# Kernel optimization log

Measured on AMD Instinct MI355X. Metric: run time of the kernel, lower is better.

## Reference

```python
import jax, jax.numpy as jnp
import numpy as np

H = W = 64
ALPHA = 1.0
BETA = 100.0
LIMB_PAIRS = np.array([[0,1],[1,2],[2,3],[0,4],[4,5],[5,6],[0,7],[7,8],[8,9],[9,10],
                       [8,11],[11,12],[12,13],[8,14],[14,15],[15,16]])
P0 = LIMB_PAIRS[:, 0]
P1 = LIMB_PAIRS[:, 1]
_last = {}
for _l, _j in enumerate(P0):
    _last[int(_j)] = _l
J0 = np.array(list(_last.keys()))   # unique proximal joints
L0 = np.array(list(_last.values())) # last limb writing to each joint


def make_kernel(h, w, alpha):
    # replicates: coords = stack(meshgrid(arange(2h-1), arange(2w-1))).transpose(1,2) (h==w)
    ii, jj = jnp.meshgrid(jnp.arange(2 * h - 1), jnp.arange(2 * w - 1), indexing='ij')
    ker = jnp.stack([h - jj, w - ii], axis=0).astype(jnp.float32)  # (2, 2h-1, 2w-1)
    dist = jnp.linalg.norm(ker, axis=0, keepdims=True)
    dist = dist.at[0, h, w].set(1.0)
    return ker / dist ** (1.0 + alpha)


def corr_full(x, k):
    # x: (N, Cin, h, w); k: (Cout, Cin, 2h-1, 2w-1); 'same' correlation with pad h-1/w-1
    h, w = x.shape[-2:]
    return jax.lax.conv_general_dilated(x, k, (1, 1), ((h - 1, h - 1), (w - 1, w - 1)))


def heatmap_std(x, di=False):
    axes = (3, 4, 5) if di else (3, 4)
    return jnp.std(x, axis=axes, keepdims=True, ddof=1)


def heatmap_normalize(x, std, di=False):
    return x * std / (heatmap_std(x, di) + 1e-6)


def l2norm(v, axis):
    return v / jnp.maximum(jnp.linalg.norm(v, axis=axis, keepdims=True), 1e-12)


def soft_argmax(hm, beta):
    # hm: ... x h x w -> ... x 2 with (row_coord, col_coord) as in the torch code
    h, w = hm.shape[-2:]
    p = jax.nn.softmax(hm.reshape(hm.shape[:-2] + (-1,)) * beta, axis=-1).reshape(hm.shape)
    rows = jnp.arange(h, dtype=p.dtype)[:, None]
    cols = jnp.arange(w, dtype=p.dtype)[None, :]
    norm = p.sum((-2, -1))
    kp_x = (p * rows).sum((-2, -1)) / norm
    kp_y = (p * cols).sum((-2, -1)) / norm
    return jnp.stack((kp_x, kp_y), axis=-1)


def scale_pts(pts, image_shape, h, w):
    return jnp.stack((pts[..., 0] * image_shape[1] / w,
                      pts[..., 1] * image_shape[0] / h), axis=-1)


def cofix_forward(heatmaps, fields, Ps, Rs, Cs, image_shape, confs, vth1, vth2, pth1, pth2):
    bs, nv, nL, _, h, w = fields.shape
    nJ = heatmaps.shape[2]
    K = make_kernel(h, w, ALPHA)  # (2, 2h-1, 2w-1)

    heatmaps = heatmaps - jnp.mean(heatmaps, axis=(3, 4), keepdims=True)
    std_hm = heatmap_std(heatmaps, di=False)
    std_df = heatmap_std(fields, di=True)

    Hs = heatmaps[:, :, P1] - heatmaps[:, :, P0]  # (bs, nv, nL, h, w)
    # conv3d(kernel1, flipped Hs) == 'same' correlation of Hs with spatially-reversed K
    k1 = K[:, ::-1, ::-1][:, None]  # (2, 1, 2h-1, 2w-1)
    convs = corr_full(Hs.reshape(-1, 1, h, w), k1).reshape(bs, nv, nL, 2, h, w)

    coef = jax.nn.relu(jnp.sum(convs * fields[..., :2, :, :], axis=3, keepdims=True))
    fields_new = fields * coef

    fnorm = jnp.linalg.norm(fields, axis=3, keepdims=True)
    lvecs = l2norm(jnp.sum(fnorm * fields, axis=(4, 5)), axis=3)
    lpts = scale_pts(soft_argmax(fnorm[:, :, :, 0], BETA), image_shape, h, w)

    fnorm_new = jnp.linalg.norm(fields_new, axis=3, keepdims=True)
    lvecs_new = l2norm(jnp.sum(fnorm_new * fields_new, axis=(4, 5)), axis=3)
    lpts_new = scale_pts(soft_argmax(fnorm_new[:, :, :, 0], BETA), image_shape, h, w)

    # original code computes vec_selection(...) then overwrites: delta[:] = 0
    delta = jnp.zeros((bs, nv, nL, 1), dtype=heatmaps.dtype)
    comb_v = delta * lvecs_new + (1 - delta) * lvecs
    comb_p = delta * lpts_new + (1 - delta) * lpts

    d6 = delta[..., None, None]
    fields_c = heatmap_normalize(fields * (1 - d6) + fields_new * d6, std_df, di=True)

    # conv2d(kernel2, fields) then output spatial flip == 'same' correlation with K
    k2 = K[None]  # (1, 2, 2h-1, 2w-1)
    fds2jts = corr_full(fields_c[..., :2, :, :].reshape(-1, 2, h, w), k2)
    fds2jts = fds2jts.reshape(bs, nv, nL, h, w)
    prox_ = jax.nn.relu(-fds2jts)
    dist_ = jax.nn.relu(fds2jts)

    hms_new = heatmaps.at[:, :, J0].set(heatmaps[:, :, J0] * prox_[:, :, L0])
    hms_new = hms_new.at[:, :, P1].set(hms_new[:, :, P1] * dist_)
    hms_new = heatmap_normalize(hms_new, std_hm, di=False)

    kps = scale_pts(soft_argmax(heatmaps, BETA), image_shape, h, w)[..., None]
    kps_new = scale_pts(soft_argmax(hms_new, BETA), image_shape, h, w)[..., None]
    kps_new = jnp.where(jnp.isnan(kps_new), kps, kps_new)

    # sed_selection (reconstructed): keep refined kps where joint conf is high and
    # the refinement displacement is small.
    confs_j = confs[:, :, nL:]
    disp = jnp.linalg.norm((kps_new - kps)[..., 0], axis=-1)  # (bs, nv, nJ)
    sel = ((confs_j > pth1) & (disp < pth2)).astype(kps.dtype)[..., None, None]
    kps_combined = sel * kps_new + (1 - sel) * kps

    return kps_combined, comb_v, comb_p, fields_new, hms_new


def setup_inputs() -> dict:
    key = jax.random.key(0)
    ks = jax.random.split(key, 6)
    bs, nv, nJ, nL = 4, 4, 17, 16
    return {
        'heatmaps': jax.random.uniform(ks[0], (bs, nv, nJ, H, W), jnp.float32),
        'fields': jax.random.normal(ks[1], (bs, nv, nL, 3, H, W), jnp.float32),
        'Ps': jax.random.normal(ks[2], (bs, nv, 3, 4), jnp.float32),
        'Rs': jax.random.normal(ks[3], (bs, nv, 3, 3), jnp.float32),
        'Cs': jax.random.normal(ks[4], (bs, nv, 3, 1), jnp.float32),
        'image_shape': jnp.array([384, 384], jnp.int32),
        'confs': jax.random.uniform(ks[5], (bs, nv, nL + nJ), jnp.float32),
        'vth1': 0.5, 'vth2': 0.5, 'pth1': 0.1, 'pth2': 20.0,
    }


def reference(heatmaps, fields, Ps, Rs, Cs, image_shape, confs, vth1, vth2, pth1, pth2):
    return cofix_forward(heatmaps, fields, Ps, Rs, Cs, image_shape, confs,
                         vth1, vth2, pth1, pth2)
```

## Files before the change

kernel.cpp:

```cpp
#include <hip/hip_runtime.h>
#include <math.h>

#define TPB 1024
#define HTPB 256
#define NPIX 4096
#define NJ 17
#define NL 16
static constexpr float kBeta = 100.0f;
static constexpr float S2H = 0.70710678118654752f;

#define O_KPS 0
#define O_CV 544
#define O_CP 1312
#define O_FN 1824
#define O_HM 3147552
#define W_FDS 0
#define W_MEAN 1048576
#define W_STD 1048848
#define W_SF 1049120
#define W_W1 1049376
#define W_W2 1082144

__device__ __constant__ int c_P0[16] = {0,1,2,0,4,5,0,7,8,9,8,11,12,8,14,15};
__device__ __constant__ int c_P1[16] = {1,2,3,4,5,6,7,8,9,10,11,12,13,14,15,16};
__device__ __constant__ int c_proxL[17] = {6,1,2,-1,4,5,-1,7,13,9,-1,11,12,-1,14,15,-1};
__device__ __constant__ int c_distL[17] = {-1,0,1,2,3,4,5,6,7,8,9,10,11,12,13,14,15};

using cplx = float2;
__device__ inline cplx cadd(cplx a, cplx b){ return {a.x+b.x, a.y+b.y}; }
__device__ inline cplx csub(cplx a, cplx b){ return {a.x-b.x, a.y-b.y}; }
__device__ inline cplx cmul(cplx a, cplx w){ return {a.x*w.x - a.y*w.y, a.x*w.y + a.y*w.x}; }
__device__ inline cplx cmulc(cplx a, cplx w){ return {a.x*w.x + a.y*w.y, a.y*w.x - a.x*w.y}; }

__device__ inline void wsync(){
  asm volatile("s_waitcnt lgkmcnt(0)" ::: "memory");
}

__device__ __constant__ float2 W128BR[8] = {
  {1.f,0.f},
  {0.98078528040323044913f,-0.19509032201612826785f},
  {0.99518472667219688624f,-0.09801714032956060199f},
  {0.95694033573220886494f,-0.29028467725446236764f},
  {0.99879545620517239271f,-0.04906767432741801425f},
  {0.97003125319454399260f,-0.24298017990326388995f},
  {0.98917650996478097345f,-0.14673047445536175166f},
  {0.94154406518302077841f,-0.33688985339222005069f}
};
__device__ __constant__ float2 W16BR[8] = {
  {1.f,0.f},
  {0.f,-1.f},
  {0.70710678118654752440f,-0.70710678118654752440f},
  {-0.70710678118654752440f,-0.70710678118654752440f},
  {0.92387953251128675613f,-0.38268343236508977173f},
  {-0.38268343236508977173f,-0.92387953251128675613f},
  {0.38268343236508977173f,-0.92387953251128675613f},
  {-0.92387953251128675613f,-0.38268343236508977173f}
};

__device__ inline void bf8_tail(cplx t0, cplx t1, cplx t2, cplx t3,
                                cplx t4, cplx t5, cplx t6, cplx t7, cplx x[8]){
  cplx u0=cadd(t0,t2), u2=csub(t0,t2);
  cplx u1=cadd(t1,t3), d13=csub(t1,t3);
  cplx u3={d13.y,-d13.x};
  cplx u4=cadd(t4,t6), u6=csub(t4,t6);
  cplx u5=cadd(t5,t7), d57=csub(t5,t7);
  cplx u7={d57.y,-d57.x};
  x[0]=cadd(u0,u1); x[1]=csub(u0,u1);
  x[2]=cadd(u2,u3); x[3]=csub(u2,u3);
  x[4]=cadd(u4,u5); x[5]=csub(u4,u5);
  x[6]=cadd(u6,u7); x[7]=csub(u6,u7);
}
__device__ inline void bf8_fwd(cplx x[8]){
  cplx t0=cadd(x[0],x[4]), d4=csub(x[0],x[4]);
  cplx t1=cadd(x[1],x[5]), d5=csub(x[1],x[5]);
  cplx t2=cadd(x[2],x[6]), d6=csub(x[2],x[6]);
  cplx t3=cadd(x[3],x[7]), d7=csub(x[3],x[7]);
  cplx t5={S2H*(d5.x+d5.y), S2H*(d5.y-d5.x)};
  cplx t6={d6.y,-d6.x};
  cplx t7={S2H*(d7.y-d7.x), -S2H*(d7.x+d7.y)};
  bf8_tail(t0,t1,t2,t3,d4,t5,t6,t7,x);
}
__device__ inline void bf8_fwd_z(cplx x[8]){
  cplx t5={S2H*(x[1].x+x[1].y), S2H*(x[1].y-x[1].x)};
  cplx t6={x[2].y,-x[2].x};
  cplx t7={S2H*(x[3].y-x[3].x), -S2H*(x[3].x+x[3].y)};
  bf8_tail(x[0],x[1],x[2],x[3],x[0],t5,t6,t7,x);
}
__device__ inline void bf8_inv(cplx y[8]){
  cplx u0=cadd(y[0],y[1]), u1=csub(y[0],y[1]);
  cplx u2=cadd(y[2],y[3]), u3=csub(y[2],y[3]);
  cplx u4=cadd(y[4],y[5]), u5=csub(y[4],y[5]);
  cplx u6=cadd(y[6],y[7]), u7=csub(y[6],y[7]);
  cplx t0=cadd(u0,u2), t2=csub(u0,u2);
  cplx iu3={-u3.y,u3.x};
  cplx t1=cadd(u1,iu3), t3=csub(u1,iu3);
  cplx t4=cadd(u4,u6), t6=csub(u4,u6);
  cplx iu7={-u7.y,u7.x};
  cplx t5=cadd(u5,iu7), t7=csub(u5,iu7);
  y[0]=cadd(t0,t4); y[4]=csub(t0,t4);
  cplx w5={S2H*(t5.x-t5.y), S2H*(t5.x+t5.y)};
  y[1]=cadd(t1,w5); y[5]=csub(t1,w5);
  cplx w6={-t6.y,t6.x};
  y[2]=cadd(t2,w6); y[6]=csub(t2,w6);
  cplx w7={-S2H*(t7.x+t7.y), S2H*(t7.x-t7.y)};
  y[3]=cadd(t3,w7); y[7]=csub(t3,w7);
}

__device__ inline void fft16_fwd(cplx z[16]){
  cplx e[8], o[8];
  #pragma unroll
  for (int t=0;t<8;t++){ e[t]=z[2*t]; o[t]=z[2*t+1]; }
  bf8_fwd(e); bf8_fwd(o);
  #pragma unroll
  for (int p=0;p<8;p++){
    cplx vo = cmul(o[p], W16BR[p]);
    z[2*p]   = cadd(e[p], vo);
    z[2*p+1] = csub(e[p], vo);
  }
}
__device__ inline void fft16_inv(cplx z[16]){
  cplx e[8], o[8];
  #pragma unroll
  for (int p=0;p<8;p++){
    cplx a=z[2*p], b=z[2*p+1];
    e[p] = cadd(a,b);
    o[p] = cmulc(csub(a,b), W16BR[p]);
  }
  bf8_inv(e); bf8_inv(o);
  #pragma unroll
  for (int t=0;t<8;t++){ z[2*t]=e[t]; z[2*t+1]=o[t]; }
}

__device__ inline void twchainA(const cplx* TW, int j, cplx A[8]){
  cplx W1 = TW[j];
  cplx W2 = cmul(W1,W1);
  cplx W4 = cmul(W2,W2);
  cplx W6 = cmul(W4,W2);
  A[0] = {1.f,0.f}; A[1] = W4; A[2] = W2; A[3] = W6;
  A[4] = W1; A[5] = cmul(W4,W1); A[6] = cmul(W2,W1); A[7] = cmul(W6,W1);
}

__device__ inline int PH(int y, int m){
  return (y<<6) | ((m ^ ((y&7)*9) ^ ((y>>3)&7)) & 63);
}

template<bool ZT>
__device__ inline void row_s1_f(float4* S4, const cplx* TW, int L, int m){
  cplx xe[8], xo[8];
  #pragma unroll
  for (int t=0; t<(ZT?4:8); t++){
    float4 v = S4[PH(L, m+8*t)];
    xe[t]={v.x,v.y}; xo[t]={v.z,v.w};
  }
  if (ZT){ bf8_fwd_z(xe); bf8_fwd_z(xo); } else { bf8_fwd(xe); bf8_fwd(xo); }
  cplx A[8]; twchainA(TW, 2*m, A);
  #pragma unroll
  for (int p=0;p<8;p++){
    cplx B = cmul(A[p], W128BR[p]);
    cplx ve = cmul(xe[p], A[p]);
    cplx vo = cmul(xo[p], B);
    S4[PH(L, m+8*p)] = {ve.x, ve.y, vo.x, vo.y};
  }
}
__device__ inline void row_s1_i(float4* S4, const cplx* TW, int L, int m){
  cplx xe[8], xo[8];
  #pragma unroll
  for (int p=0;p<8;p++){
    float4 v = S4[PH(L, m+8*p)];
    xe[p]={v.x,v.y}; xo[p]={v.z,v.w};
  }
  cplx A[8]; twchainA(TW, 2*m, A);
  #pragma unroll
  for (int p=0;p<8;p++){
    cplx B = cmul(A[p], W128BR[p]);
    xe[p] = cmulc(xe[p], A[p]);
    xo[p] = cmulc(xo[p], B);
  }
  bf8_inv(xe); bf8_inv(xo);
  #pragma unroll
  for (int t=0;t<4;t++)
    S4[PH(L, m+8*t)] = {xe[t].x, xe[t].y, xo[t].x, xo[t].y};
}
__device__ inline void row_s2_f(float4* S4, int L, int jb){
  cplx z[16];
  #pragma unroll
  for (int k=0;k<8;k++){
    float4 v = S4[PH(L, jb*8+k)];
    z[2*k]={v.x,v.y}; z[2*k+1]={v.z,v.w};
  }
  fft16_fwd(z);
  #pragma unroll
  for (int k=0;k<8;k++)
    S4[PH(L, jb*8+k)] = {z[2*k].x, z[2*k].y, z[2*k+1].x, z[2*k+1].y};
}
__device__ inline void row_s2_i(float4* S4, int L, int jb){
  cplx z[16];
  #pragma unroll
  for (int k=0;k<8;k++){
    float4 v = S4[PH(L, jb*8+k)];
    z[2*k]={v.x,v.y}; z[2*k+1]={v.z,v.w};
  }
  fft16_inv(z);
  #pragma unroll
  for (int k=0;k<8;k++)
    S4[PH(L, jb*8+k)] = {z[2*k].x, z[2*k].y, z[2*k+1].x, z[2*k+1].y};
}
template<bool ZT>
__device__ inline void col_s1_f(float4* S4, const cplx* TW, int yj, int sc){
  cplx xe[8], xo[8];
  #pragma unroll
  for (int t=0; t<(ZT?4:8); t++){
    float4 v = S4[PH(yj+16*t, sc)];
    xe[t]={v.x,v.y}; xo[t]={v.z,v.w};
  }
  if (ZT){ bf8_fwd_z(xe); bf8_fwd_z(xo); } else { bf8_fwd(xe); bf8_fwd(xo); }
  cplx A[8]; twchainA(TW, yj, A);
  #pragma unroll
  for (int p=0;p<8;p++){
    cplx ve = cmul(xe[p], A[p]);
    cplx vo = cmul(xo[p], A[p]);
    S4[PH(yj+16*p, sc)] = {ve.x, ve.y, vo.x, vo.y};
  }
}
__device__ inline void col_s1_i(float4* S4, const cplx* TW, int yj, int sc){
  cplx xe[8], xo[8];
  #pragma unroll
  for (int p=0;p<8;p++){
    float4 v = S4[PH(yj+16*p, sc)];
    xe[p]={v.x,v.y}; xo[p]={v.z,v.w};
  }
  cplx A[8]; twchainA(TW, yj, A);
  #pragma unroll
  for (int p=0;p<8;p++){
    xe[p] = cmulc(xe[p], A[p]);
    xo[p] = cmulc(xo[p], A[p]);
  }
  bf8_inv(xe); bf8_inv(xo);
  #pragma unroll
  for (int t=0;t<4;t++)
    S4[PH(yj+16*t, sc)] = {xe[t].x, xe[t].y, xo[t].x, xo[t].y};
}

__device__ inline float wred(float v){
  #pragma unroll
  for (int o=32;o;o>>=1) v += __shfl_xor(v, o, 64);
  return v;
}
__device__ inline float wredmax(float v){
  #pragma unroll
  for (int o=32;o;o>>=1) v = fmaxf(v, __shfl_xor(v, o, 64));
  return v;
}
template<int NW>
__device__ inline void bred3(float& a, float& b, float& c,
                             float* s0, float* s1, float* s2, int tid){
  a = wred(a); b = wred(b); c = wred(c);
  const int w = tid >> 6;
  if ((tid & 63) == 0){ s0[w]=a; s1[w]=b; s2[w]=c; }
  __syncthreads();
  if (tid == 0){
    float A=0.f, B=0.f, C=0.f;
    #pragma unroll
    for (int i=0;i<NW;i++){ A+=s0[i]; B+=s1[i]; C+=s2[i]; }
    s0[0]=A; s1[0]=B; s2[0]=C;
  }
  __syncthreads();
  a = s0[0]; b = s1[0]; c = s2[0];
  __syncthreads();
}
template<int NW>
__device__ inline float bredmax(float v, float* s0, int tid){
  v = wredmax(v);
  const int w = tid >> 6;
  if ((tid & 63) == 0) s0[w] = v;
  __syncthreads();
  if (tid == 0){
    float M = s0[0];
    #pragma unroll
    for (int i=1;i<NW;i++) M = fmaxf(M, s0[i]);
    s0[0] = M;
  }
  __syncthreads();
  const float r = s0[0];
  __syncthreads();
  return r;
}

__device__ inline cplx wval(int r, int c, int which){
  const int dy = (r<64)? r : r-128;
  const int dx = (c<64)? c : c-128;
  float a, b;
  if (which==0){ a = 1.f-(float)dy; b = 1.f-(float)dx; }
  else         { a = 1.f+(float)dy; b = 1.f+(float)dx; }
  const float den = a*a + b*b;
  if (r==64 || c==64 || den<=0.f) return {0.f,0.f};
  const float inv = 1.f/den;
  return {a*inv, -b*inv};
}

__global__ __launch_bounds__(TPB,4) void pre_kernel(const float* __restrict__ heat,
                                                    const float* __restrict__ fields,
                                                    const int* __restrict__ ishape,
                                                    float* __restrict__ mean_hm,
                                                    float* __restrict__ std_hm,
                                                    float* __restrict__ sf,
                                                    float* __restrict__ W1,
                                                    float* __restrict__ W2,
                                                    float* __restrict__ out){
  __shared__ float4 S4[8192];
  __shared__ cplx TW[128];
  __shared__ float sA[16], sB[16], sC[16];
  const int tid = threadIdx.x;
  const int wv = tid >> 6, lane = tid & 63;
  const int blk = blockIdx.x;
  if (blk < 2){
    const int which = blk;
    if (tid < 128){
      float s, c;
      sincosf(-6.283185307179586f * (float)tid / 128.0f, &s, &c);
      TW[tid] = {c, s};
    }
    for (int s = tid; s < 8192; s += TPB){
      const int y = s>>6, m = s&63;
      const cplx v0 = wval(y, 2*m, which);
      const cplx v1 = wval(y, 2*m+1, which);
      S4[PH(y, m)] = {v0.x, v0.y, v1.x, v1.y};
    }
    __syncthreads();
    {
      const int L = 8*wv + (lane>>3), m = lane&7;
      row_s1_f<false>(S4, TW, L, m);
      wsync();
      row_s2_f(S4, L, m);
    }
    __syncthreads();
    {
      const int yj = lane & 15, sc = 4*wv + (lane>>4);
      col_s1_f<false>(S4, TW, yj, sc);
      wsync();
      cplx* Sc = (cplx*)S4;
      const int c = 8*wv + (lane&7), r = lane>>3;
      cplx z[16];
      #pragma unroll
      for (int i=0;i<16;i++)
        z[i] = Sc[2*PH(16*r+i, c>>1) + (c&1)];
      fft16_fwd(z);
      cplx* Wo = (cplx*)((which==0)?W1:W2);
      const float scl = 1.0f / 16384.0f;
      #pragma unroll
      for (int i=0;i<16;i++) Wo[(16*r+i)*128 + c] = {z[i].x*scl, z[i].y*scl};
    }
  } else if (blk < 274){
    const int n = blk - 2;
    const float4* p4 = (const float4*)(heat + (size_t)n * NPIX);
    const float4 x = p4[tid];
    float s = x.x+x.y+x.z+x.w;
    float s2 = x.x*x.x + x.y*x.y + x.z*x.z + x.w*x.w;
    float d = 0.0f;
    bred3<16>(s, s2, d, sA, sB, sC, tid);
    if (tid == 0){
      const float mean = s / 4096.0f;
      const float var = (s2 - s*mean) / 4095.0f;
      mean_hm[n] = mean;
      std_hm[n] = sqrtf(fmaxf(var, 0.0f));
    }
  } else {
    const int m = blk - 274;
    const float4* F4 = (const float4*)(fields + (size_t)m * 3 * NPIX);
    const float4 f0 = F4[tid], f1 = F4[1024+tid], f2 = F4[2048+tid];
    const float f0a[4] = {f0.x,f0.y,f0.z,f0.w};
    const float f1a[4] = {f1.x,f1.y,f1.z,f1.w};
    const float f2a[4] = {f2.x,f2.y,f2.z,f2.w};
    float fn[4];
    float s1 = 0.0f, s2 = 0.0f;
    float a0 = 0.0f, a1 = 0.0f, a2 = 0.0f;
    #pragma unroll
    for (int j = 0; j < 4; j++){
      s1 += f0a[j]+f1a[j]+f2a[j];
      s2 += f0a[j]*f0a[j]+f1a[j]*f1a[j]+f2a[j]*f2a[j];
      const float nn = sqrtf(f0a[j]*f0a[j] + f1a[j]*f1a[j] + f2a[j]*f2a[j]);
      fn[j] = nn;
      a0 += nn*f0a[j]; a1 += nn*f1a[j]; a2 += nn*f2a[j];
    }
    {
      float t1 = s1, t2 = s2, t3 = 0.0f;
      bred3<16>(t1, t2, t3, sA, sB, sC, tid);
      if (tid == 0){
        const float var = (t2 - t1*t1/12288.0f) / 12287.0f;
        const float sd = sqrtf(fmaxf(var, 0.0f));
        sf[m] = sd / (sd + 1e-6f);
      }
    }
    bred3<16>(a0, a1, a2, sA, sB, sC, tid);
    float mx = fmaxf(fmaxf(fn[0],fn[1]), fmaxf(fn[2],fn[3]));
    mx = bredmax<16>(mx, sA, tid);
    float Sm = 0.0f, Sx = 0.0f, Sy = 0.0f;
    #pragma unroll
    for (int j = 0; j < 4; j++){
      const int px = tid*4 + j;
      const float e = expf(kBeta * (fn[j] - mx));
      Sm += e; Sx += e * (float)(px>>6); Sy += e * (float)(px&63);
    }
    bred3<16>(Sm, Sx, Sy, sA, sB, sC, tid);
    if (tid == 0){
      float nrm = sqrtf(a0*a0 + a1*a1 + a2*a2);
      nrm = fmaxf(nrm, 1e-12f);
      out[O_CV + m*3 + 0] = a0/nrm;
      out[O_CV + m*3 + 1] = a1/nrm;
      out[O_CV + m*3 + 2] = a2/nrm;
      const float sxs = (float)ishape[1] / 64.0f;
      const float sys = (float)ishape[0] / 64.0f;
      out[O_CP + m*2 + 0] = Sx/Sm * sxs;
      out[O_CP + m*2 + 1] = Sy/Sm * sys;
    }
  }
}

__global__ __launch_bounds__(TPB,4) void conv_kernel(const float* __restrict__ heat,
                                                     const float* __restrict__ mean_hm,
                                                     const float* __restrict__ fields,
                                                     const float* __restrict__ sf,
                                                     const float* __restrict__ W1g,
                                                     const float* __restrict__ W2g,
                                                     float* __restrict__ out_fn,
                                                     float* __restrict__ fds){
  __shared__ float4 S4[8192];
  __shared__ cplx TW[128];
  const int tid = threadIdx.x;
  const int wv = tid >> 6, lane = tid & 63;
  const int n = blockIdx.x;
  const bool is2 = (n < 256);
  const int m_img = is2 ? n : (n - 256);
  if (tid < 128){
    float s, c;
    sincosf(-6.283185307179586f * (float)tid / 128.0f, &s, &c);
    TW[tid] = {c, s};
  }
  const float* f = fields + (size_t)m_img * 3 * NPIX;
  {
    const int y = tid >> 4, x4 = (tid & 15) << 2;
    const int i = (y << 6) + x4;
    const int m = (tid & 15) << 1;
    if (!is2){
      const int bv = m_img >> 4, l = m_img & 15;
      const int j1 = bv*NJ + c_P1[l], j0 = bv*NJ + c_P0[l];
      const float dm = mean_hm[j1] - mean_hm[j0];
      const float4 a = *(const float4*)(heat + (size_t)j1*NPIX + i);
      const float4 b = *(const float4*)(heat + (size_t)j0*NPIX + i);
      S4[PH(y, m  )] = {a.x-b.x-dm, 0.f, a.y-b.y-dm, 0.f};
      S4[PH(y, m+1)] = {a.z-b.z-dm, 0.f, a.w-b.w-dm, 0.f};
    } else {
      const float4 A = *(const float4*)(f + NPIX + i);
      const float4 B = *(const float4*)(f + i);
      S4[PH(y, m  )] = {A.x, B.x, A.y, B.y};
      S4[PH(y, m+1)] = {A.z, B.z, A.w, B.w};
    }
  }
  __syncthreads();
  if (wv < 8){
    const int L = 8*wv + (lane>>3), m = lane&7;
    row_s1_f<true>(S4, TW, L, m);
    wsync();
    row_s2_f(S4, L, m);
  }
  __syncthreads();
  {
    const cplx* Wg = (const cplx*)(is2 ? W2g : W1g);
    const int c = 8*wv + (lane&7), r = lane>>3;
    cplx wvv[16];
    #pragma unroll
    for (int i=0;i<16;i++) wvv[i] = Wg[(16*r+i)*128 + c];
    const int yj = lane & 15, sc = 4*wv + (lane>>4);
    col_s1_f<true>(S4, TW, yj, sc);
    wsync();
    {
      cplx* Sc = (cplx*)S4;
      cplx z[16];
      int ad[16];
      #pragma unroll
      for (int i=0;i<16;i++){
        ad[i] = 2*PH(16*r+i, c>>1) + (c&1);
        z[i] = Sc[ad[i]];
      }
      fft16_fwd(z);
      #pragma unroll
      for (int i=0;i<16;i++) z[i] = cmul(z[i], wvv[i]);
      fft16_inv(z);
      #pragma unroll
      for (int i=0;i<16;i++) Sc[ad[i]] = z[i];
    }
    wsync();
    col_s1_i(S4, TW, yj, sc);
  }
  __syncthreads();
  if (wv < 8){
    const int L = 8*wv + (lane>>3), m = lane&7;
    row_s2_i(S4, L, m);
    wsync();
    row_s1_i(S4, TW, L, m);
  }
  __syncthreads();
  {
    const int y = tid >> 4, x4 = (tid & 15) << 2;
    const int i = (y << 6) + x4;
    const int m = (tid & 15) << 1;
    const float4 va = S4[PH(y, m)];
    const float4 vb = S4[PH(y, m+1)];
    if (!is2){
      float* o = out_fn + (size_t)m_img * 3 * NPIX;
      const float4 f0 = *(const float4*)(f + i);
      const float4 f1 = *(const float4*)(f + NPIX + i);
      const float4 f2 = *(const float4*)(f + 2*NPIX + i);
      const float c0[4] = {-va.y, -va.w, -vb.y, -vb.w};
      const float c1[4] = { va.x,  va.z,  vb.x,  vb.z};
      const float f0a[4] = {f0.x,f0.y,f0.z,f0.w};
      const float f1a[4] = {f1.x,f1.y,f1.z,f1.w};
      const float f2a[4] = {f2.x,f2.y,f2.z,f2.w};
      float o0[4], o1[4], o2[4];
      #pragma unroll
      for (int j=0;j<4;j++){
        const float cf = fmaxf(0.f, c0[j]*f0a[j] + c1[j]*f1a[j]);
        o0[j] = f0a[j]*cf; o1[j] = f1a[j]*cf; o2[j] = f2a[j]*cf;
      }
      *(float4*)(o + i)          = {o0[0],o0[1],o0[2],o0[3]};
      *(float4*)(o + NPIX + i)   = {o1[0],o1[1],o1[2],o1[3]};
      *(float4*)(o + 2*NPIX + i) = {o2[0],o2[1],o2[2],o2[3]};
    } else {
      const float sc2 = sf[m_img];
      float* o = fds + (size_t)m_img * NPIX;
      *(float4*)(o + i) = {va.x*sc2, va.z*sc2, vb.x*sc2, vb.z*sc2};
    }
  }
}

__global__ __launch_bounds__(HTPB) void hms_kernel(const float* __restrict__ heat,
                                                   const float* __restrict__ mean_hm,
                                                   const float* __restrict__ std_hm,
                                                   const float* __restrict__ fds,
                                                   const float* __restrict__ confs,
                                                   const int* __restrict__ ishape,
                                                   const float* __restrict__ pth1p,
                                                   const float* __restrict__ pth2p,
                                                   float* __restrict__ out){
  __shared__ float sA[4], sB[4], sC[4];
  const int tid = threadIdx.x;
  const int idx = blockIdx.x;
  const int bv = idx / NJ, j = idx % NJ;
  const float4* hp4 = (const float4*)(heat + (size_t)idx * NPIX);
  const float mh = mean_hm[idx];
  const int pl = c_proxL[j], dl = c_distL[j];
  const float4* fp4 = (pl >= 0) ? (const float4*)(fds + (size_t)(bv*NL + pl) * NPIX) : nullptr;
  const float4* fd4 = (dl >= 0) ? (const float4*)(fds + (size_t)(bv*NL + dl) * NPIX) : nullptr;
  float ho[16], hn[16];
  float s = 0.0f, s2 = 0.0f, dummy = 0.0f;
  #pragma unroll
  for (int i = 0; i < 4; i++){
    const int u = tid + i*HTPB;
    const float4 h4 = hp4[u];
    const float hv[4] = {h4.x-mh, h4.y-mh, h4.z-mh, h4.w-mh};
    float pv[4] = {1.f,1.f,1.f,1.f};
    if (pl >= 0){
      const float4 p4 = fp4[u];
      pv[0] = fmaxf(0.f,-p4.x); pv[1] = fmaxf(0.f,-p4.y);
      pv[2] = fmaxf(0.f,-p4.z); pv[3] = fmaxf(0.f,-p4.w);
    }
    float dv[4] = {1.f,1.f,1.f,1.f};
    if (dl >= 0){
      const float4 d4 = fd4[u];
      dv[0] = fmaxf(0.f,d4.x); dv[1] = fmaxf(0.f,d4.y);
      dv[2] = fmaxf(0.f,d4.z); dv[3] = fmaxf(0.f,d4.w);
    }
    #pragma unroll
    for (int k=0;k<4;k++){
      ho[4*i+k] = hv[k];
      const float m = hv[k]*pv[k]*dv[k];
      hn[4*i+k] = m;
      s += m; s2 += m*m;
    }
  }
  bred3<4>(s, s2, dummy, sA, sB, sC, tid);
  const float var = (s2 - s*s/4096.0f) / 4095.0f;
  const float sdn = sqrtf(fmaxf(var, 0.0f));
  const float scale = std_hm[idx] / (sdn + 1e-6f);
  float4* ohm4 = (float4*)(out + O_HM + (size_t)idx * NPIX);
  #pragma unroll
  for (int i = 0; i < 4; i++){
    #pragma unroll
    for (int k=0;k<4;k++) hn[4*i+k] *= scale;
    ohm4[tid + i*HTPB] = {hn[4*i], hn[4*i+1], hn[4*i+2], hn[4*i+3]};
  }
  float mo = -1e30f, mn = -1e30f;
  #pragma unroll
  for (int i = 0; i < 16; i++){ mo = fmaxf(mo, ho[i]); mn = fmaxf(mn, hn[i]); }
  mo = bredmax<4>(mo, sA, tid);
  mn = bredmax<4>(mn, sA, tid);
  float So = 0.0f, Sxo = 0.0f, Syo = 0.0f;
  float Sn = 0.0f, Sxn = 0.0f, Syn = 0.0f;
  #pragma unroll
  for (int i = 0; i < 16; i++){
    const int px = (tid + (i>>2)*HTPB)*4 + (i&3);
    const float y = (float)(px >> 6), x = (float)(px & 63);
    const float eo = expf(kBeta * (ho[i] - mo));
    So += eo; Sxo += eo*y; Syo += eo*x;
    const float en = expf(kBeta * (hn[i] - mn));
    Sn += en; Sxn += en*y; Syn += en*x;
  }
  bred3<4>(So, Sxo, Syo, sA, sB, sC, tid);
  bred3<4>(Sn, Sxn, Syn, sA, sB, sC, tid);
  if (tid == 0){
    const float sxs = (float)ishape[1] / 64.0f;
    const float sys = (float)ishape[0] / 64.0f;
    const float kxo = Sxo/So * sxs, kyo = Syo/So * sys;
    float kxn = Sxn/Sn * sxs, kyn = Syn/Sn * sys;
    if (kxn != kxn) kxn = kxo;
    if (kyn != kyn) kyn = kyo;
    const float ddx = kxn - kxo, ddy = kyn - kyo;
    const float disp = sqrtf(ddx*ddx + ddy*ddy);
    const float conf = confs[bv*(NL+NJ) + NL + j];
    const bool sel = (conf > pth1p[0]) && (disp < pth2p[0]);
    out[O_KPS + idx*2 + 0] = sel ? kxn : kxo;
    out[O_KPS + idx*2 + 1] = sel ? kyn : kyo;
  }
}

extern "C" void kernel_launch(void* const* d_in, const int* in_sizes, int n_in,
                              void* d_out, int out_size, void* d_ws, size_t ws_size,
                              hipStream_t stream) {
  const float* heat   = (const float*)d_in[0];
  const float* fields = (const float*)d_in[1];
  const int*   ishape = (const int*)d_in[5];
  const float* confs  = (const float*)d_in[6];
  const float* pth1   = (const float*)d_in[9];
  const float* pth2   = (const float*)d_in[10];
  float* out = (float*)d_out;
  float* ws = (float*)d_ws;
  float* fds     = ws + W_FDS;
  float* mean_hm = ws + W_MEAN;
  float* std_hm  = ws + W_STD;
  float* sf      = ws + W_SF;
  float* W1      = ws + W_W1;
  float* W2      = ws + W_W2;

  hipLaunchKernelGGL(pre_kernel, dim3(530), dim3(TPB), 0, stream,
                     heat, fields, ishape, mean_hm, std_hm, sf, W1, W2, out);
  hipLaunchKernelGGL(conv_kernel, dim3(512), dim3(TPB), 0, stream,
                     heat, mean_hm, fields, sf, W1, W2, out + O_FN, fds);
  hipLaunchKernelGGL(hms_kernel, dim3(272), dim3(HTPB), 0, stream,
                     heat, mean_hm, std_hm, fds, confs, ishape, pth1, pth2, out);
}
```

Before: 142.8 us.

## Fold per-image statistics into conv and heatmap kernels, shrink pre-kernel

Removes the heatmap mean/std and field statistics work from the first kernel and recomputes them inside the consumers: conv_kernel computes the difference mean and the field std via block reductions, and takes over the field-norm soft-argmax and combined-vector outputs. hms_kernel computes its own heatmap mean and std with an extra reduction pass. The first kernel now only builds the two FFT weight grids in two blocks, which shortens the serial critical path and drops the workspace round trips. In exchange conv and hms blocks carry extra reductions and syncs, and the z-channel of each field is loaded one more time.

```diff
diff --git a/kernel.cpp b/kernel.cpp
--- a/kernel.cpp
+++ b/kernel.cpp
@@ -15,9 +15,6 @@
 #define O_FN 1824
 #define O_HM 3147552
 #define W_FDS 0
-#define W_MEAN 1048576
-#define W_STD 1048848
-#define W_SF 1049120
 #define W_W1 1049376
 #define W_W2 1082144
 
@@ -252,6 +249,23 @@
   return v;
 }
 template<int NW>
+__device__ inline float bred1(float v, float* s0, int tid){
+  v = wred(v);
+  const int w = tid >> 6;
+  if ((tid & 63) == 0) s0[w] = v;
+  __syncthreads();
+  if (tid == 0){
+    float A = 0.f;
+    #pragma unroll
+    for (int i=0;i<NW;i++) A += s0[i];
+    s0[0] = A;
+  }
+  __syncthreads();
+  const float r = s0[0];
+  __syncthreads();
+  return r;
+}
+template<int NW>
 __device__ inline void bred3(float& a, float& b, float& c,
                              float* s0, float* s1, float* s2, int tid){
   a = wred(a); b = wred(b); c = wred(c);
@@ -298,134 +312,60 @@
   return {a*inv, -b*inv};
 }
 
-__global__ __launch_bounds__(TPB,4) void pre_kernel(const float* __restrict__ heat,
-                                                    const float* __restrict__ fields,
-                                                    const int* __restrict__ ishape,
-                                                    float* __restrict__ mean_hm,
-                                                    float* __restrict__ std_hm,
-                                                    float* __restrict__ sf,
-                                                    float* __restrict__ W1,
-                                                    float* __restrict__ W2,
-                                                    float* __restrict__ out){
+__global__ __launch_bounds__(TPB,4) void prep_kernel(float* __restrict__ W1,
+                                                     float* __restrict__ W2){
+  __shared__ float4 S4[8192];
+  __shared__ cplx TW[128];
+  const int tid = threadIdx.x;
+  const int wvx = tid >> 6, lane = tid & 63;
+  const int which = blockIdx.x;
+  if (tid < 128){
+    float s, c;
+    sincosf(-6.283185307179586f * (float)tid / 128.0f, &s, &c);
+    TW[tid] = {c, s};
+  }
+  for (int s = tid; s < 8192; s += TPB){
+    const int y = s>>6, m = s&63;
+    const cplx v0 = wval(y, 2*m, which);
+    const cplx v1 = wval(y, 2*m+1, which);
+    S4[PH(y, m)] = {v0.x, v0.y, v1.x, v1.y};
+  }
+  __syncthreads();
+  {
+    const int L = 8*wvx + (lane>>3), m = lane&7;
+    row_s1_f<false>(S4, TW, L, m);
+    wsync();
+    row_s2_f(S4, L, m);
+  }
+  __syncthreads();
+  {
+    const int yj = lane & 15, sc = 4*wvx + (lane>>4);
+    col_s1_f<false>(S4, TW, yj, sc);
+    wsync();
+    cplx* Sc = (cplx*)S4;
+    const int c = 8*wvx + (lane&7), r = lane>>3;
+    cplx z[16];
+    #pragma unroll
+    for (int i=0;i<16;i++)
+      z[i] = Sc[2*PH(16*r+i, c>>1) + (c&1)];
+    fft16_fwd(z);
+    cplx* Wo = (cplx*)((which==0)?W1:W2);
+    const float scl = 1.0f / 16384.0f;
+    #pragma unroll
+    for (int i=0;i<16;i++) Wo[(16*r+i)*128 + c] = {z[i].x*scl, z[i].y*scl};
+  }
+}
+
+__global__ __launch_bounds__(TPB,4) void conv_kernel(const float* __restrict__ heat,
+                                                     const float* __restrict__ fields,
+                                                     const float* __restrict__ W1g,
+                                                     const float* __restrict__ W2g,
+                                                     const int* __restrict__ ishape,
+                                                     float* __restrict__ out,
+                                                     float* __restrict__ fds){
   __shared__ float4 S4[8192];
   __shared__ cplx TW[128];
   __shared__ float sA[16], sB[16], sC[16];
-  const int tid = threadIdx.x;
-  const int wv = tid >> 6, lane = tid & 63;
-  const int blk = blockIdx.x;
-  if (blk < 2){
-    const int which = blk;
-    if (tid < 128){
-      float s, c;
-      sincosf(-6.283185307179586f * (float)tid / 128.0f, &s, &c);
-      TW[tid] = {c, s};
-    }
-    for (int s = tid; s < 8192; s += TPB){
-      const int y = s>>6, m = s&63;
-      const cplx v0 = wval(y, 2*m, which);
-      const cplx v1 = wval(y, 2*m+1, which);
-      S4[PH(y, m)] = {v0.x, v0.y, v1.x, v1.y};
-    }
-    __syncthreads();
-    {
-      const int L = 8*wv + (lane>>3), m = lane&7;
-      row_s1_f<false>(S4, TW, L, m);
-      wsync();
-      row_s2_f(S4, L, m);
-    }
-    __syncthreads();
-    {
-      const int yj = lane & 15, sc = 4*wv + (lane>>4);
-      col_s1_f<false>(S4, TW, yj, sc);
-      wsync();
-      cplx* Sc = (cplx*)S4;
-      const int c = 8*wv + (lane&7), r = lane>>3;
-      cplx z[16];
-      #pragma unroll
-      for (int i=0;i<16;i++)
-        z[i] = Sc[2*PH(16*r+i, c>>1) + (c&1)];
-      fft16_fwd(z);
-      cplx* Wo = (cplx*)((which==0)?W1:W2);
-      const float scl = 1.0f / 16384.0f;
-      #pragma unroll
-      for (int i=0;i<16;i++) Wo[(16*r+i)*128 + c] = {z[i].x*scl, z[i].y*scl};
-    }
-  } else if (blk < 274){
-    const int n = blk - 2;
-    const float4* p4 = (const float4*)(heat + (size_t)n * NPIX);
-    const float4 x = p4[tid];
-    float s = x.x+x.y+x.z+x.w;
-    float s2 = x.x*x.x + x.y*x.y + x.z*x.z + x.w*x.w;
-    float d = 0.0f;
-    bred3<16>(s, s2, d, sA, sB, sC, tid);
-    if (tid == 0){
-      const float mean = s / 4096.0f;
-      const float var = (s2 - s*mean) / 4095.0f;
-      mean_hm[n] = mean;
-      std_hm[n] = sqrtf(fmaxf(var, 0.0f));
-    }
-  } else {
-    const int m = blk - 274;
-    const float4* F4 = (const float4*)(fields + (size_t)m * 3 * NPIX);
-    const float4 f0 = F4[tid], f1 = F4[1024+tid], f2 = F4[2048+tid];
-    const float f0a[4] = {f0.x,f0.y,f0.z,f0.w};
-    const float f1a[4] = {f1.x,f1.y,f1.z,f1.w};
-    const float f2a[4] = {f2.x,f2.y,f2.z,f2.w};
-    float fn[4];
-    float s1 = 0.0f, s2 = 0.0f;
-    float a0 = 0.0f, a1 = 0.0f, a2 = 0.0f;
-    #pragma unroll
-    for (int j = 0; j < 4; j++){
-      s1 += f0a[j]+f1a[j]+f2a[j];
-      s2 += f0a[j]*f0a[j]+f1a[j]*f1a[j]+f2a[j]*f2a[j];
-      const float nn = sqrtf(f0a[j]*f0a[j] + f1a[j]*f1a[j] + f2a[j]*f2a[j]);
-      fn[j] = nn;
-      a0 += nn*f0a[j]; a1 += nn*f1a[j]; a2 += nn*f2a[j];
-    }
-    {
-      float t1 = s1, t2 = s2, t3 = 0.0f;
-      bred3<16>(t1, t2, t3, sA, sB, sC, tid);
-      if (tid == 0){
-        const float var = (t2 - t1*t1/12288.0f) / 12287.0f;
-        const float sd = sqrtf(fmaxf(var, 0.0f));
-        sf[m] = sd / (sd + 1e-6f);
-      }
-    }
-    bred3<16>(a0, a1, a2, sA, sB, sC, tid);
-    float mx = fmaxf(fmaxf(fn[0],fn[1]), fmaxf(fn[2],fn[3]));
-    mx = bredmax<16>(mx, sA, tid);
-    float Sm = 0.0f, Sx = 0.0f, Sy = 0.0f;
-    #pragma unroll
-    for (int j = 0; j < 4; j++){
-      const int px = tid*4 + j;
-      const float e = expf(kBeta * (fn[j] - mx));
-      Sm += e; Sx += e * (float)(px>>6); Sy += e * (float)(px&63);
-    }
-    bred3<16>(Sm, Sx, Sy, sA, sB, sC, tid);
-    if (tid == 0){
-      float nrm = sqrtf(a0*a0 + a1*a1 + a2*a2);
-      nrm = fmaxf(nrm, 1e-12f);
-      out[O_CV + m*3 + 0] = a0/nrm;
-      out[O_CV + m*3 + 1] = a1/nrm;
-      out[O_CV + m*3 + 2] = a2/nrm;
-      const float sxs = (float)ishape[1] / 64.0f;
-      const float sys = (float)ishape[0] / 64.0f;
-      out[O_CP + m*2 + 0] = Sx/Sm * sxs;
-      out[O_CP + m*2 + 1] = Sy/Sm * sys;
-    }
-  }
-}
-
-__global__ __launch_bounds__(TPB,4) void conv_kernel(const float* __restrict__ heat,
-                                                     const float* __restrict__ mean_hm,
-                                                     const float* __restrict__ fields,
-                                                     const float* __restrict__ sf,
-                                                     const float* __restrict__ W1g,
-                                                     const float* __restrict__ W2g,
-                                                     float* __restrict__ out_fn,
-                                                     float* __restrict__ fds){
-  __shared__ float4 S4[8192];
-  __shared__ cplx TW[128];
   const int tid = threadIdx.x;
   const int wv = tid >> 6, lane = tid & 63;
   const int n = blockIdx.x;
@@ -437,31 +377,41 @@
     TW[tid] = {c, s};
   }
   const float* f = fields + (size_t)m_img * 3 * NPIX;
-  {
-    const int y = tid >> 4, x4 = (tid & 15) << 2;
-    const int i = (y << 6) + x4;
-    const int m = (tid & 15) << 1;
-    if (!is2){
-      const int bv = m_img >> 4, l = m_img & 15;
-      const int j1 = bv*NJ + c_P1[l], j0 = bv*NJ + c_P0[l];
-      const float dm = mean_hm[j1] - mean_hm[j0];
-      const float4 a = *(const float4*)(heat + (size_t)j1*NPIX + i);
-      const float4 b = *(const float4*)(heat + (size_t)j0*NPIX + i);
-      S4[PH(y, m  )] = {a.x-b.x-dm, 0.f, a.y-b.y-dm, 0.f};
-      S4[PH(y, m+1)] = {a.z-b.z-dm, 0.f, a.w-b.w-dm, 0.f};
-    } else {
-      const float4 A = *(const float4*)(f + NPIX + i);
-      const float4 B = *(const float4*)(f + i);
-      S4[PH(y, m  )] = {A.x, B.x, A.y, B.y};
-      S4[PH(y, m+1)] = {A.z, B.z, A.w, B.w};
-    }
+  const int y = tid >> 4, x4 = (tid & 15) << 2;
+  const int i = (y << 6) + x4;
+  const int m = (tid & 15) << 1;
+  float sf_loc = 0.0f;
+  if (!is2){
+    const int bv = m_img >> 4, l = m_img & 15;
+    const int j1 = bv*NJ + c_P1[l], j0 = bv*NJ + c_P0[l];
+    const float4 a = *(const float4*)(heat + (size_t)j1*NPIX + i);
+    const float4 b = *(const float4*)(heat + (size_t)j0*NPIX + i);
+    const float d0=a.x-b.x, d1=a.y-b.y, d2=a.z-b.z, d3=a.w-b.w;
+    const float dm = bred1<16>(d0+d1+d2+d3, sA, tid) * (1.0f/4096.0f);
+    S4[PH(y, m  )] = {d0-dm, 0.f, d1-dm, 0.f};
+    S4[PH(y, m+1)] = {d2-dm, 0.f, d3-dm, 0.f};
+  } else {
+    const float4 A = *(const float4*)(f + NPIX + i);
+    const float4 B = *(const float4*)(f + i);
+    const float4 C = *(const float4*)(f + 2*NPIX + i);
+    S4[PH(y, m  )] = {A.x, B.x, A.y, B.y};
+    S4[PH(y, m+1)] = {A.z, B.z, A.w, B.w};
+    float s1 = A.x+A.y+A.z+A.w + B.x+B.y+B.z+B.w + C.x+C.y+C.z+C.w;
+    float s2 = A.x*A.x+A.y*A.y+A.z*A.z+A.w*A.w
+             + B.x*B.x+B.y*B.y+B.z*B.z+B.w*B.w
+             + C.x*C.x+C.y*C.y+C.z*C.z+C.w*C.w;
+    float d = 0.0f;
+    bred3<16>(s1, s2, d, sA, sB, sC, tid);
+    const float var = (s2 - s1*s1/12288.0f) / 12287.0f;
+    const float sd = sqrtf(fmaxf(var, 0.0f));
+    sf_loc = sd / (sd + 1e-6f);
   }
   __syncthreads();
   if (wv < 8){
-    const int L = 8*wv + (lane>>3), m = lane&7;
-    row_s1_f<true>(S4, TW, L, m);
+    const int L = 8*wv + (lane>>3), mm = lane&7;
+    row_s1_f<true>(S4, TW, L, mm);
     wsync();
-    row_s2_f(S4, L, m);
+    row_s2_f(S4, L, mm);
   }
   __syncthreads();
   {
@@ -469,7 +419,7 @@
     const int c = 8*wv + (lane&7), r = lane>>3;
     cplx wvv[16];
     #pragma unroll
-    for (int i=0;i<16;i++) wvv[i] = Wg[(16*r+i)*128 + c];
+    for (int k=0;k<16;k++) wvv[k] = Wg[(16*r+k)*128 + c];
     const int yj = lane & 15, sc = 4*wv + (lane>>4);
     col_s1_f<true>(S4, TW, yj, sc);
     wsync();
@@ -478,64 +428,81 @@
       cplx z[16];
       int ad[16];
       #pragma unroll
-      for (int i=0;i<16;i++){
-        ad[i] = 2*PH(16*r+i, c>>1) + (c&1);
-        z[i] = Sc[ad[i]];
+      for (int k=0;k<16;k++){
+        ad[k] = 2*PH(16*r+k, c>>1) + (c&1);
+        z[k] = Sc[ad[k]];
       }
       fft16_fwd(z);
       #pragma unroll
-      for (int i=0;i<16;i++) z[i] = cmul(z[i], wvv[i]);
+      for (int k=0;k<16;k++) z[k] = cmul(z[k], wvv[k]);
       fft16_inv(z);
       #pragma unroll
-      for (int i=0;i<16;i++) Sc[ad[i]] = z[i];
+      for (int k=0;k<16;k++) Sc[ad[k]] = z[k];
     }
     wsync();
     col_s1_i(S4, TW, yj, sc);
   }
   __syncthreads();
   if (wv < 8){
-    const int L = 8*wv + (lane>>3), m = lane&7;
-    row_s2_i(S4, L, m);
+    const int L = 8*wv + (lane>>3), mm = lane&7;
+    row_s2_i(S4, L, mm);
     wsync();
-    row_s1_i(S4, TW, L, m);
-  }
-  __syncthreads();
-  {
-    const int y = tid >> 4, x4 = (tid & 15) << 2;
-    const int i = (y << 6) + x4;
-    const int m = (tid & 15) << 1;
-    const float4 va = S4[PH(y, m)];
-    const float4 vb = S4[PH(y, m+1)];
-    if (!is2){
-      float* o = out_fn + (size_t)m_img * 3 * NPIX;
-      const float4 f0 = *(const float4*)(f + i);
-      const float4 f1 = *(const float4*)(f + NPIX + i);
-      const float4 f2 = *(const float4*)(f + 2*NPIX + i);
-      const float c0[4] = {-va.y, -va.w, -vb.y, -vb.w};
-      const float c1[4] = { va.x,  va.z,  vb.x,  vb.z};
-      const float f0a[4] = {f0.x,f0.y,f0.z,f0.w};
-      const float f1a[4] = {f1.x,f1.y,f1.z,f1.w};
-      const float f2a[4] = {f2.x,f2.y,f2.z,f2.w};
-      float o0[4], o1[4], o2[4];
-      #pragma unroll
-      for (int j=0;j<4;j++){
-        const float cf = fmaxf(0.f, c0[j]*f0a[j] + c1[j]*f1a[j]);
-        o0[j] = f0a[j]*cf; o1[j] = f1a[j]*cf; o2[j] = f2a[j]*cf;
-      }
-      *(float4*)(o + i)          = {o0[0],o0[1],o0[2],o0[3]};
-      *(float4*)(o + NPIX + i)   = {o1[0],o1[1],o1[2],o1[3]};
-      *(float4*)(o + 2*NPIX + i) = {o2[0],o2[1],o2[2],o2[3]};
-    } else {
-      const float sc2 = sf[m_img];
-      float* o = fds + (size_t)m_img * NPIX;
-      *(float4*)(o + i) = {va.x*sc2, va.z*sc2, vb.x*sc2, vb.z*sc2};
+    row_s1_i(S4, TW, L, mm);
+  }
+  __syncthreads();
+  const float4 va = S4[PH(y, m)];
+  const float4 vb = S4[PH(y, m+1)];
+  if (!is2){
+    float* o = out + O_FN + (size_t)m_img * 3 * NPIX;
+    const float4 f0 = *(const float4*)(f + i);
+    const float4 f1 = *(const float4*)(f + NPIX + i);
+    const float4 f2 = *(const float4*)(f + 2*NPIX + i);
+    const float c0[4] = {-va.y, -va.w, -vb.y, -vb.w};
+    const float c1[4] = { va.x,  va.z,  vb.x,  vb.z};
+    const float f0a[4] = {f0.x,f0.y,f0.z,f0.w};
+    const float f1a[4] = {f1.x,f1.y,f1.z,f1.w};
+    const float f2a[4] = {f2.x,f2.y,f2.z,f2.w};
+    float o0[4], o1[4], o2[4], fn[4];
+    float a0 = 0.f, a1 = 0.f, a2 = 0.f;
+    #pragma unroll
+    for (int j=0;j<4;j++){
+      const float cf = fmaxf(0.f, c0[j]*f0a[j] + c1[j]*f1a[j]);
+      o0[j] = f0a[j]*cf; o1[j] = f1a[j]*cf; o2[j] = f2a[j]*cf;
+      const float nn = sqrtf(f0a[j]*f0a[j] + f1a[j]*f1a[j] + f2a[j]*f2a[j]);
+      fn[j] = nn;
+      a0 += nn*f0a[j]; a1 += nn*f1a[j]; a2 += nn*f2a[j];
     }
+    *(float4*)(o + i)          = {o0[0],o0[1],o0[2],o0[3]};
+    *(float4*)(o + NPIX + i)   = {o1[0],o1[1],o1[2],o1[3]};
+    *(float4*)(o + 2*NPIX + i) = {o2[0],o2[1],o2[2],o2[3]};
+    bred3<16>(a0, a1, a2, sA, sB, sC, tid);
+    float mx = fmaxf(fmaxf(fn[0],fn[1]), fmaxf(fn[2],fn[3]));
+    mx = bredmax<16>(mx, sA, tid);
+    float Sm = 0.f, Sx = 0.f, Sy = 0.f;
+    #pragma unroll
+    for (int j=0;j<4;j++){
+      const float e = expf(kBeta * (fn[j] - mx));
+      Sm += e; Sx += e * (float)y; Sy += e * (float)(x4 + j);
+    }
+    bred3<16>(Sm, Sx, Sy, sA, sB, sC, tid);
+    if (tid == 0){
+      float nrm = sqrtf(a0*a0 + a1*a1 + a2*a2);
+      nrm = fmaxf(nrm, 1e-12f);
+      out[O_CV + m_img*3 + 0] = a0/nrm;
+      out[O_CV + m_img*3 + 1] = a1/nrm;
+      out[O_CV + m_img*3 + 2] = a2/nrm;
+      const float sxs = (float)ishape[1] / 64.0f;
+      const float sys = (float)ishape[0] / 64.0f;
+      out[O_CP + m_img*2 + 0] = Sx/Sm * sxs;
+      out[O_CP + m_img*2 + 1] = Sy/Sm * sys;
+    }
+  } else {
+    float* o = fds + (size_t)m_img * NPIX;
+    *(float4*)(o + i) = {va.x*sf_loc, va.z*sf_loc, vb.x*sf_loc, vb.z*sf_loc};
   }
 }
 
 __global__ __launch_bounds__(HTPB) void hms_kernel(const float* __restrict__ heat,
-                                                   const float* __restrict__ mean_hm,
-                                                   const float* __restrict__ std_hm,
                                                    const float* __restrict__ fds,
                                                    const float* __restrict__ confs,
                                                    const int* __restrict__ ishape,
@@ -547,17 +514,16 @@
   const int idx = blockIdx.x;
   const int bv = idx / NJ, j = idx % NJ;
   const float4* hp4 = (const float4*)(heat + (size_t)idx * NPIX);
-  const float mh = mean_hm[idx];
   const int pl = c_proxL[j], dl = c_distL[j];
   const float4* fp4 = (pl >= 0) ? (const float4*)(fds + (size_t)(bv*NL + pl) * NPIX) : nullptr;
   const float4* fd4 = (dl >= 0) ? (const float4*)(fds + (size_t)(bv*NL + dl) * NPIX) : nullptr;
-  float ho[16], hn[16];
+  float ho[16], prod[16];
   float s = 0.0f, s2 = 0.0f, dummy = 0.0f;
   #pragma unroll
   for (int i = 0; i < 4; i++){
     const int u = tid + i*HTPB;
     const float4 h4 = hp4[u];
-    const float hv[4] = {h4.x-mh, h4.y-mh, h4.z-mh, h4.w-mh};
+    const float hv[4] = {h4.x, h4.y, h4.z, h4.w};
     float pv[4] = {1.f,1.f,1.f,1.f};
     if (pl >= 0){
       const float4 p4 = fp4[u];
@@ -573,15 +539,26 @@
     #pragma unroll
     for (int k=0;k<4;k++){
       ho[4*i+k] = hv[k];
-      const float m = hv[k]*pv[k]*dv[k];
-      hn[4*i+k] = m;
-      s += m; s2 += m*m;
+      prod[4*i+k] = pv[k]*dv[k];
+      s += hv[k]; s2 += hv[k]*hv[k];
     }
   }
   bred3<4>(s, s2, dummy, sA, sB, sC, tid);
-  const float var = (s2 - s*s/4096.0f) / 4095.0f;
-  const float sdn = sqrtf(fmaxf(var, 0.0f));
-  const float scale = std_hm[idx] / (sdn + 1e-6f);
+  const float mh = s / 4096.0f;
+  const float sdh = sqrtf(fmaxf((s2 - s*mh) / 4095.0f, 0.0f));
+  float hn[16];
+  float sn = 0.0f, sn2 = 0.0f; dummy = 0.0f;
+  #pragma unroll
+  for (int i = 0; i < 16; i++){
+    ho[i] -= mh;
+    const float mm = ho[i]*prod[i];
+    hn[i] = mm;
+    sn += mm; sn2 += mm*mm;
+  }
+  bred3<4>(sn, sn2, dummy, sA, sB, sC, tid);
+  const float varn = (sn2 - sn*sn/4096.0f) / 4095.0f;
+  const float sdn = sqrtf(fmaxf(varn, 0.0f));
+  const float scale = sdh / (sdn + 1e-6f);
   float4* ohm4 = (float4*)(out + O_HM + (size_t)idx * NPIX);
   #pragma unroll
   for (int i = 0; i < 4; i++){
@@ -599,11 +576,11 @@
   #pragma unroll
   for (int i = 0; i < 16; i++){
     const int px = (tid + (i>>2)*HTPB)*4 + (i&3);
-    const float y = (float)(px >> 6), x = (float)(px & 63);
+    const float yy = (float)(px >> 6), xx = (float)(px & 63);
     const float eo = expf(kBeta * (ho[i] - mo));
-    So += eo; Sxo += eo*y; Syo += eo*x;
+    So += eo; Sxo += eo*yy; Syo += eo*xx;
     const float en = expf(kBeta * (hn[i] - mn));
-    Sn += en; Sxn += en*y; Syn += en*x;
+    Sn += en; Sxn += en*yy; Syn += en*xx;
   }
   bred3<4>(So, Sxo, Syo, sA, sB, sC, tid);
   bred3<4>(Sn, Sxn, Syn, sA, sB, sC, tid);
@@ -634,17 +611,13 @@
   const float* pth2   = (const float*)d_in[10];
   float* out = (float*)d_out;
   float* ws = (float*)d_ws;
-  float* fds     = ws + W_FDS;
-  float* mean_hm = ws + W_MEAN;
-  float* std_hm  = ws + W_STD;
-  float* sf      = ws + W_SF;
-  float* W1      = ws + W_W1;
-  float* W2      = ws + W_W2;
-
-  hipLaunchKernelGGL(pre_kernel, dim3(530), dim3(TPB), 0, stream,
-                     heat, fields, ishape, mean_hm, std_hm, sf, W1, W2, out);
+  float* fds = ws + W_FDS;
+  float* W1  = ws + W_W1;
+  float* W2  = ws + W_W2;
+
+  hipLaunchKernelGGL(prep_kernel, dim3(2), dim3(TPB), 0, stream, W1, W2);
   hipLaunchKernelGGL(conv_kernel, dim3(512), dim3(TPB), 0, stream,
-                     heat, mean_hm, fields, sf, W1, W2, out + O_FN, fds);
+                     heat, fields, W1, W2, ishape, out, fds);
   hipLaunchKernelGGL(hms_kernel, dim3(272), dim3(HTPB), 0, stream,
-                     heat, mean_hm, std_hm, fds, confs, ishape, pth1, pth2, out);
-}
+                     heat, fds, confs, ishape, pth1, pth2, out);
+}
```

Result: slower. 147.8 us (+3.5%).
